# Kernel tuning notes

Hardware: AMD Instinct MI355X
Metric: run time of the kernel (lower is better)

## Reference

```python
import jax, jax.numpy as jnp
import numpy as np


def setup_inputs() -> dict:
    key = jax.random.key(0)
    B, L, H, D = 4, 4096, 8, 64
    sample_k = int(np.ceil(np.log(L)))  # factor=1 -> U_part = ceil(ln L_K) = 9
    k1, k2, k3, k4 = jax.random.split(key, 4)
    return {
        "queries": jax.random.normal(k1, (B, L, H, D), jnp.float32),
        "keys": jax.random.normal(k2, (B, L, H, D), jnp.float32),
        "values": jax.random.normal(k3, (B, L, H, D), jnp.float32),
        "index_sample": jax.random.randint(k4, (L, sample_k), 0, L),
    }


def _prob_attention(Q, K, V, index_sample):
    # Q, K, V: [B, H, L, D]
    B, H, L_K, D = K.shape
    L_Q = Q.shape[2]
    u = min(int(np.ceil(np.log(L_Q))), L_Q)  # n_top (static)

    # --- _prob_QK: sampled scores, sparsity measure M, top-u queries ---
    # gather sampled keys per query position: [B, H, L_Q, sample_k, D]
    K_sample = K[:, :, index_sample, :]
    QK_sample = jnp.einsum('bhld,bhlsd->bhls', Q, K_sample)  # [B,H,L_Q,S]
    M = QK_sample.max(axis=-1) - QK_sample.sum(axis=-1) / L_K  # [B,H,L_Q]
    _, M_top = jax.lax.top_k(M, u)  # [B,H,u] indices of top queries

    Q_reduce = jnp.take_along_axis(Q, M_top[..., None], axis=2)  # [B,H,u,D]
    scale = 1.0 / jnp.sqrt(jnp.asarray(D, Q.dtype))
    scores = jnp.einsum('bhud,bhkd->bhuk', Q_reduce, K) * scale  # [B,H,u,L_K]

    # --- initial context (mask_flag=False): mean of V over keys ---
    context = jnp.broadcast_to(V.mean(axis=2, keepdims=True), (B, H, L_Q, D))

    # --- update context at the top-u query positions ---
    attn = jax.nn.softmax(scores, axis=-1)  # [B,H,u,L_K]
    ctx_top = jnp.einsum('bhuk,bhkd->bhud', attn, V)  # [B,H,u,D]
    b_idx = jnp.arange(B)[:, None, None]
    h_idx = jnp.arange(H)[None, :, None]
    context = context.at[b_idx, h_idx, M_top].set(ctx_top)
    return context, attn


def reference(queries, keys, values, index_sample):
    # inputs: [B, L, H, D] -> internal [B, H, L, D]
    Q = queries.transpose(0, 2, 1, 3)
    K = keys.transpose(0, 2, 1, 3)
    V = values.transpose(0, 2, 1, 3)
    context, attn = _prob_attention(Q, K, V, index_sample)
    return context.transpose(0, 2, 1, 3), attn
```

## Files before the change

kernel.cpp:

```cpp
#include <hip/hip_runtime.h>
#include <math.h>

#define B_ 4
#define L_ 4096
#define H_ 8
#define D_ 64
#define S_ 9
#define U_ 9
#define VC_ 64
#define NC_ 32
#define CC_ 16
#define TKC_ 8

#define MBLK_ 2048
#define FILLBLK_ 8192

__device__ __forceinline__ float dot4(const float4& a, const float4& b) {
    return a.x * b.x + a.y * b.y + a.z * b.z + a.w * b.w;
}

__global__ void kernel_M_vmean(const float* __restrict__ Q, const float* __restrict__ K,
                               const int* __restrict__ idx, float* __restrict__ M,
                               const float* __restrict__ V, float* __restrict__ vpart) {
    if (blockIdx.x >= MBLK_) {
        int blk = blockIdx.x - MBLK_;
        int c = blk & (VC_ - 1), b = blk >> 6;
        int col = threadIdx.x & 127;
        int lp  = threadIdx.x >> 7;
        const int CHUNK = L_ / VC_;
        const float4* base = (const float4*)(V + (size_t)b * L_ * H_ * D_);
        float4 acc = make_float4(0.f, 0.f, 0.f, 0.f);
        for (int l = c * CHUNK + lp; l < (c + 1) * CHUNK; l += 2) {
            float4 v = base[(size_t)l * 128 + col];
            acc.x += v.x; acc.y += v.y; acc.z += v.z; acc.w += v.w;
        }
        __shared__ float4 red[256];
        red[threadIdx.x] = acc;
        __syncthreads();
        if (lp == 0) {
            float4 o = red[threadIdx.x + 128];
            acc.x += o.x; acc.y += o.y; acc.z += o.z; acc.w += o.w;
            ((float4*)vpart)[(size_t)blk * 128 + col] = acc;
        }
        return;
    }
    int n = blockIdx.x;
    int x = n & 7, m = n >> 3;
    int chunk = m & 63;
    int bh = (m >> 6) * 8 + x;
    int h = bh & (H_ - 1), b = bh >> 3;
    int t = threadIdx.x;
    int j = t & 3;
    int l = chunk * 64 + (t >> 2);

    int ki[S_];
#pragma unroll
    for (int s = 0; s < S_; ++s) ki[s] = idx[l * S_ + s];

    const float4* qb = (const float4*)(Q + (size_t)((b * L_ + l) * H_ + h) * D_);
    float4 q[4];
#pragma unroll
    for (int c = 0; c < 4; ++c) q[c] = qb[j + 4 * c];

    float dot[S_];
#pragma unroll
    for (int r = 0; r < 3; ++r) {
        const float4* kb0 = (const float4*)(K + (size_t)((b * L_ + ki[3*r+0]) * H_ + h) * D_);
        const float4* kb1 = (const float4*)(K + (size_t)((b * L_ + ki[3*r+1]) * H_ + h) * D_);
        const float4* kb2 = (const float4*)(K + (size_t)((b * L_ + ki[3*r+2]) * H_ + h) * D_);
        float4 kv0[4], kv1[4], kv2[4];
#pragma unroll
        for (int c = 0; c < 4; ++c) {
            kv0[c] = kb0[j + 4 * c];
            kv1[c] = kb1[j + 4 * c];
            kv2[c] = kb2[j + 4 * c];
        }
        float a0 = 0.f, a1 = 0.f, a2 = 0.f;
#pragma unroll
        for (int c = 0; c < 4; ++c) {
            a0 += dot4(q[c], kv0[c]);
            a1 += dot4(q[c], kv1[c]);
            a2 += dot4(q[c], kv2[c]);
        }
        dot[3*r+0] = a0; dot[3*r+1] = a1; dot[3*r+2] = a2;
    }
#pragma unroll
    for (int s = 0; s < S_; ++s) {
        dot[s] += __shfl_xor(dot[s], 1);
        dot[s] += __shfl_xor(dot[s], 2);
    }
    if (j == 0) {
        float mx = -INFINITY, sm = 0.f;
#pragma unroll
        for (int s = 0; s < S_; ++s) { mx = fmaxf(mx, dot[s]); sm += dot[s]; }
        M[((size_t)bh << 12) + l] = mx - sm * (1.0f / (float)L_);
    }
}

#define CSWAP(a, b)                                                          \
    if (v[b] > v[a] || (v[b] == v[a] && id[b] < id[a])) {                    \
        float tv = v[a]; v[a] = v[b]; v[b] = tv;                             \
        int ti = id[a]; id[a] = id[b]; id[b] = ti;                           \
    }

__global__ void kernel_topk1(const float* __restrict__ M,
                             float* __restrict__ cand_v, int* __restrict__ cand_i) {
    int bh = blockIdx.x >> 3;
    int chunk = blockIdx.x & (TKC_ - 1);
    int lane = threadIdx.x;
    const float* Ms = M + ((size_t)bh << 12);

    float v[8]; int id[8];
#pragma unroll
    for (int c = 0; c < 8; ++c) {
        int gi = chunk * 512 + lane + 64 * c;
        v[c] = Ms[gi]; id[c] = gi;
    }
    CSWAP(0,1) CSWAP(2,3) CSWAP(4,5) CSWAP(6,7)
    CSWAP(0,2) CSWAP(1,3) CSWAP(4,6) CSWAP(5,7)
    CSWAP(1,2) CSWAP(5,6)
    CSWAP(0,4) CSWAP(1,5) CSWAP(2,6) CSWAP(3,7)
    CSWAP(2,4) CSWAP(3,5)
    CSWAP(1,2) CSWAP(3,4) CSWAP(5,6)

    float* cv = cand_v + (size_t)blockIdx.x * U_;
    int*   ci = cand_i + (size_t)blockIdx.x * U_;
#pragma unroll
    for (int r = 0; r < U_; ++r) {
        float bv = v[0]; int bi = id[0];
#pragma unroll
        for (int off = 1; off < 64; off <<= 1) {
            float ov = __shfl_xor(bv, off);
            int   oi = __shfl_xor(bi, off);
            if (ov > bv || (ov == bv && oi < bi)) { bv = ov; bi = oi; }
        }
        if (lane == 0) { cv[r] = bv; ci[r] = bi; }
        if (id[0] == bi) {
#pragma unroll
            for (int c = 0; c < 7; ++c) { v[c] = v[c+1]; id[c] = id[c+1]; }
            v[7] = -INFINITY; id[7] = 0x7fffffff;
        }
    }
}

__global__ void kernel_small(const float* __restrict__ cand_v, const int* __restrict__ cand_i,
                             int* __restrict__ Mtop, const float* __restrict__ vpart,
                             float* __restrict__ vmean) {
    if (blockIdx.x >= 32) {
        int bh = blockIdx.x - 32;
        int h = bh & (H_ - 1), b = bh >> 3;
        int d = threadIdx.x;
        float s = 0.0f;
        for (int c = 0; c < VC_; ++c)
            s += vpart[(size_t)(b * VC_ + c) * (H_ * D_) + h * D_ + d];
        vmean[bh * D_ + d] = s * (1.0f / (float)L_);
        return;
    }
    int bh = blockIdx.x;
    int lane = threadIdx.x;
    const float* cv = cand_v + (size_t)bh * (TKC_ * U_);
    const int*   ci = cand_i + (size_t)bh * (TKC_ * U_);

    float v[2]; int id[2];
    v[0] = cv[lane]; id[0] = ci[lane];
    if (lane < TKC_ * U_ - 64) { v[1] = cv[64 + lane]; id[1] = ci[64 + lane]; }
    else { v[1] = -INFINITY; id[1] = 0x7fffffff; }
    CSWAP(0,1)

#pragma unroll
    for (int r = 0; r < U_; ++r) {
        float bv = v[0]; int bi = id[0];
#pragma unroll
        for (int off = 1; off < 64; off <<= 1) {
            float ov = __shfl_xor(bv, off);
            int   oi = __shfl_xor(bi, off);
            if (ov > bv || (ov == bv && oi < bi)) { bv = ov; bi = oi; }
        }
        if (lane == 0) Mtop[bh * U_ + r] = bi;
        if (id[0] == bi) { v[0] = v[1]; id[0] = id[1]; v[1] = -INFINITY; id[1] = 0x7fffffff; }
    }
}

__global__ void kernel_fill_scores(float* __restrict__ out, const float* __restrict__ vmean,
                                   const float* __restrict__ Q, const float* __restrict__ K,
                                   const int* __restrict__ Mtop, float* __restrict__ raw) {
    if (blockIdx.x < FILLBLK_) {
        int i = blockIdx.x * 256 + threadIdx.x;
        int d4 = i & 15;
        int h  = (i >> 4) & (H_ - 1);
        int b  = i >> (4 + 3 + 12);
        ((float4*)out)[i] = ((const float4*)vmean)[(b * H_ + h) * 16 + d4];
        return;
    }
    int n = blockIdx.x - FILLBLK_;
    int x = n & 7, m = n >> 3;
    int chunk = m & (NC_ - 1);
    int bh = (m >> 5) * 8 + x;
    int h = bh & (H_ - 1), b = bh >> 3;
    int k0 = chunk * (L_ / NC_);

    __shared__ float qs[U_][D_];
    int t = threadIdx.x;
    if (t < 144) {
        int u = t / 16, c = t & 15;
        int l = Mtop[bh * U_ + u];
        ((float4*)qs[u])[c] =
            ((const float4*)(Q + (size_t)((b * L_ + l) * H_ + h) * D_))[c];
    }
    __syncthreads();

    int j = t & 3, g = t >> 2;
#pragma unroll
    for (int kk = 0; kk < 2; ++kk) {
        int k = k0 + g + 64 * kk;
        const float4* kb = (const float4*)(K + (size_t)((b * L_ + k) * H_ + h) * D_);
        float4 kv[4];
#pragma unroll
        for (int c = 0; c < 4; ++c) kv[c] = kb[j + 4 * c];
#pragma unroll
        for (int u = 0; u < U_; ++u) {
            float acc = 0.0f;
#pragma unroll
            for (int c = 0; c < 4; ++c)
                acc += dot4(((const float4*)qs[u])[j + 4 * c], kv[c]);
            acc += __shfl_xor(acc, 1);
            acc += __shfl_xor(acc, 2);
            if (j == 0) raw[((size_t)bh * U_ + u) * L_ + k] = acc * 0.125f;
        }
    }
}

__global__ void kernel_softmax(float* __restrict__ attn) {
    int row = blockIdx.x;
    float4* a = (float4*)(attn + (size_t)row * L_);
    int t = threadIdx.x;

    float4 v[4];
    float mx = -INFINITY;
#pragma unroll
    for (int i = 0; i < 4; ++i) {
        v[i] = a[t + 256 * i];
        mx = fmaxf(mx, fmaxf(fmaxf(v[i].x, v[i].y), fmaxf(v[i].z, v[i].w)));
    }
    __shared__ float red[256];
    __shared__ float bmax, bsum;
    red[t] = mx;
    __syncthreads();
    for (int off = 128; off > 0; off >>= 1) {
        if (t < off) red[t] = fmaxf(red[t], red[t + off]);
        __syncthreads();
    }
    if (t == 0) bmax = red[0];
    __syncthreads();

    float mm = bmax, sum = 0.0f;
#pragma unroll
    for (int i = 0; i < 4; ++i) {
        v[i].x = expf(v[i].x - mm); v[i].y = expf(v[i].y - mm);
        v[i].z = expf(v[i].z - mm); v[i].w = expf(v[i].w - mm);
        sum += v[i].x + v[i].y + v[i].z + v[i].w;
    }
    red[t] = sum;
    __syncthreads();
    for (int off = 128; off > 0; off >>= 1) {
        if (t < off) red[t] += red[t + off];
        __syncthreads();
    }
    if (t == 0) bsum = red[0];
    __syncthreads();

    float inv = 1.0f / bsum;
#pragma unroll
    for (int i = 0; i < 4; ++i) {
        v[i].x *= inv; v[i].y *= inv; v[i].z *= inv; v[i].w *= inv;
        a[t + 256 * i] = v[i];
    }
}

__global__ void kernel_ctxf(const float* __restrict__ attn, const float* __restrict__ V,
                            float* __restrict__ cpart) {
    int n = blockIdx.x;
    int x = n & 7, m = n >> 3;
    int chunk = m & (CC_ - 1);
    int bh = (m >> 4) * 8 + x;
    int h = bh & (H_ - 1), b = bh >> 3;
    int k0 = chunk * (L_ / CC_);

    int t = threadIdx.x;
    int g = t >> 6, lane = t & 63;
    int kl = lane >> 4, d4 = lane & 15;
    const float* abase = attn + (size_t)bh * U_ * L_;

    float4 acc[U_];
#pragma unroll
    for (int u = 0; u < U_; ++u) acc[u] = make_float4(0.f, 0.f, 0.f, 0.f);

    for (int i = 0; i < 16; ++i) {
        int k = k0 + (g * 4 + kl) + 16 * i;
        float4 vv = *(const float4*)(V + (size_t)((b * L_ + k) * H_ + h) * D_ + 4 * d4);
        float av[U_];
#pragma unroll
        for (int u = 0; u < U_; ++u) av[u] = abase[(size_t)u * L_ + k];
#pragma unroll
        for (int u = 0; u < U_; ++u) {
            acc[u].x += av[u] * vv.x; acc[u].y += av[u] * vv.y;
            acc[u].z += av[u] * vv.z; acc[u].w += av[u] * vv.w;
        }
    }
#pragma unroll
    for (int u = 0; u < U_; ++u) {
        acc[u].x += __shfl_xor(acc[u].x, 16); acc[u].y += __shfl_xor(acc[u].y, 16);
        acc[u].z += __shfl_xor(acc[u].z, 16); acc[u].w += __shfl_xor(acc[u].w, 16);
        acc[u].x += __shfl_xor(acc[u].x, 32); acc[u].y += __shfl_xor(acc[u].y, 32);
        acc[u].z += __shfl_xor(acc[u].z, 32); acc[u].w += __shfl_xor(acc[u].w, 32);
    }
    __shared__ float4 red[U_][4][16];
    if (kl == 0) {
#pragma unroll
        for (int u = 0; u < U_; ++u) red[u][g][d4] = acc[u];
    }
    __syncthreads();
    if (t < U_ * 16) {
        int u = t >> 4, dd = t & 15;
        float4 s0 = red[u][0][dd], s1 = red[u][1][dd];
        float4 s2 = red[u][2][dd], s3 = red[u][3][dd];
        float4 s = make_float4(s0.x + s1.x + s2.x + s3.x, s0.y + s1.y + s2.y + s3.y,
                               s0.z + s1.z + s2.z + s3.z, s0.w + s1.w + s2.w + s3.w);
        ((float4*)cpart)[((size_t)(bh * CC_ + chunk) * U_ + u) * 16 + dd] = s;
    }
}

__global__ void kernel_ctx2(const float* __restrict__ cpart, const int* __restrict__ Mtop,
                            float* __restrict__ out) {
    int row = blockIdx.x;
    int u = row % U_, bh = row / U_;
    int h = bh & (H_ - 1), b = bh >> 3;
    int d = threadIdx.x;
    float s = 0.0f;
#pragma unroll
    for (int c = 0; c < CC_; ++c)
        s += cpart[((size_t)(bh * CC_ + c) * U_ + u) * 64 + d];
    int l = Mtop[bh * U_ + u];
    out[(size_t)((b * L_ + l) * H_ + h) * D_ + d] = s;
}

extern "C" void kernel_launch(void* const* d_in, const int* in_sizes, int n_in,
                              void* d_out, int out_size, void* d_ws, size_t ws_size,
                              hipStream_t stream) {
    const float* Q   = (const float*)d_in[0];
    const float* K   = (const float*)d_in[1];
    const float* V   = (const float*)d_in[2];
    const int*   idx = (const int*)d_in[3];

    float* ctx_out  = (float*)d_out;
    float* attn_out = (float*)d_out + (size_t)B_ * L_ * H_ * D_;

    float* M      = (float*)d_ws;
    float* vpart  = M + (size_t)B_ * H_ * L_;
    float* vmean  = vpart + (size_t)B_ * VC_ * H_ * D_;
    float* cpart  = vmean + B_ * H_ * D_;
    float* cand_v = cpart + (size_t)32 * CC_ * U_ * 64;
    int*   cand_i = (int*)(cand_v + 32 * TKC_ * U_);
    int*   Mtop   = cand_i + 32 * TKC_ * U_;

    kernel_M_vmean<<<MBLK_ + B_ * VC_, 256, 0, stream>>>(Q, K, idx, M, V, vpart);
    kernel_topk1<<<B_ * H_ * TKC_, 64, 0, stream>>>(M, cand_v, cand_i);
    kernel_small<<<64, 64, 0, stream>>>(cand_v, cand_i, Mtop, vpart, vmean);
    kernel_fill_scores<<<FILLBLK_ + 32 * NC_, 256, 0, stream>>>(ctx_out, vmean, Q, K, Mtop, attn_out);
    kernel_softmax<<<B_ * H_ * U_, 256, 0, stream>>>(attn_out);
    kernel_ctxf<<<32 * CC_, 256, 0, stream>>>(attn_out, V, cpart);
    kernel_ctx2<<<B_ * H_ * U_, 64, 0, stream>>>(cpart, Mtop, ctx_out);
}
```

Before: 232.0 us.

## Split sampled-QK per sample, fuse softmax normalize into ctx, atomically scatter context

The M computation now gives each sampled key its own thread group, writing raw dot products to a workspace. The top-k kernel then reduces them to max minus sum. Softmax is split into a stats pass that writes row max and inverse sum, and the exp/normalize step moves into the context kernel. That kernel writes the normalized attention back, stages it in shared memory, and atomically adds partial contexts into the output, removing the ctx2 reduction kernel. The fill kernel now zeroes the top-u rows so the atomics accumulate from zero. Costs are extra dot-product traffic in the workspace, a 9-way Mtop compare per fill thread, and float atomics, which make the summation order nondeterministic.

```diff
diff --git a/kernel.cpp b/kernel.cpp
--- a/kernel.cpp
+++ b/kernel.cpp
@@ -12,16 +12,16 @@
 #define CC_ 16
 #define TKC_ 8
 
-#define MBLK_ 2048
+#define MBLK_ 18432
 #define FILLBLK_ 8192
 
 __device__ __forceinline__ float dot4(const float4& a, const float4& b) {
     return a.x * b.x + a.y * b.y + a.z * b.z + a.w * b.w;
 }
 
-__global__ void kernel_M_vmean(const float* __restrict__ Q, const float* __restrict__ K,
-                               const int* __restrict__ idx, float* __restrict__ M,
-                               const float* __restrict__ V, float* __restrict__ vpart) {
+__global__ void kernel_Mv(const float* __restrict__ Q, const float* __restrict__ K,
+                          const int* __restrict__ idx, float* __restrict__ dots,
+                          const float* __restrict__ V, float* __restrict__ vpart) {
     if (blockIdx.x >= MBLK_) {
         int blk = blockIdx.x - MBLK_;
         int c = blk & (VC_ - 1), b = blk >> 6;
@@ -46,55 +46,25 @@
     }
     int n = blockIdx.x;
     int x = n & 7, m = n >> 3;
-    int chunk = m & 63;
-    int bh = (m >> 6) * 8 + x;
+    int bhi = m / 576, blk = m - bhi * 576;
+    int bh = bhi * 8 + x;
     int h = bh & (H_ - 1), b = bh >> 3;
     int t = threadIdx.x;
     int j = t & 3;
-    int l = chunk * 64 + (t >> 2);
-
-    int ki[S_];
-#pragma unroll
-    for (int s = 0; s < S_; ++s) ki[s] = idx[l * S_ + s];
-
+    int G = blk * 64 + (t >> 2);
+    int s = G >> 12;
+    int l = G & (L_ - 1);
+
+    int ki = idx[l * S_ + s];
     const float4* qb = (const float4*)(Q + (size_t)((b * L_ + l) * H_ + h) * D_);
-    float4 q[4];
-#pragma unroll
-    for (int c = 0; c < 4; ++c) q[c] = qb[j + 4 * c];
-
-    float dot[S_];
-#pragma unroll
-    for (int r = 0; r < 3; ++r) {
-        const float4* kb0 = (const float4*)(K + (size_t)((b * L_ + ki[3*r+0]) * H_ + h) * D_);
-        const float4* kb1 = (const float4*)(K + (size_t)((b * L_ + ki[3*r+1]) * H_ + h) * D_);
-        const float4* kb2 = (const float4*)(K + (size_t)((b * L_ + ki[3*r+2]) * H_ + h) * D_);
-        float4 kv0[4], kv1[4], kv2[4];
-#pragma unroll
-        for (int c = 0; c < 4; ++c) {
-            kv0[c] = kb0[j + 4 * c];
-            kv1[c] = kb1[j + 4 * c];
-            kv2[c] = kb2[j + 4 * c];
-        }
-        float a0 = 0.f, a1 = 0.f, a2 = 0.f;
-#pragma unroll
-        for (int c = 0; c < 4; ++c) {
-            a0 += dot4(q[c], kv0[c]);
-            a1 += dot4(q[c], kv1[c]);
-            a2 += dot4(q[c], kv2[c]);
-        }
-        dot[3*r+0] = a0; dot[3*r+1] = a1; dot[3*r+2] = a2;
-    }
-#pragma unroll
-    for (int s = 0; s < S_; ++s) {
-        dot[s] += __shfl_xor(dot[s], 1);
-        dot[s] += __shfl_xor(dot[s], 2);
-    }
-    if (j == 0) {
-        float mx = -INFINITY, sm = 0.f;
-#pragma unroll
-        for (int s = 0; s < S_; ++s) { mx = fmaxf(mx, dot[s]); sm += dot[s]; }
-        M[((size_t)bh << 12) + l] = mx - sm * (1.0f / (float)L_);
-    }
+    const float4* kb = (const float4*)(K + (size_t)((b * L_ + ki) * H_ + h) * D_);
+
+    float acc = 0.0f;
+#pragma unroll
+    for (int c = 0; c < 4; ++c) acc += dot4(qb[j + 4 * c], kb[j + 4 * c]);
+    acc += __shfl_xor(acc, 1);
+    acc += __shfl_xor(acc, 2);
+    if (j == 0) dots[((size_t)bh * S_ + s) * L_ + l] = acc;
 }
 
 #define CSWAP(a, b)                                                          \
@@ -103,18 +73,25 @@
         int ti = id[a]; id[a] = id[b]; id[b] = ti;                           \
     }
 
-__global__ void kernel_topk1(const float* __restrict__ M,
+__global__ void kernel_topk1(const float* __restrict__ dots,
                              float* __restrict__ cand_v, int* __restrict__ cand_i) {
     int bh = blockIdx.x >> 3;
     int chunk = blockIdx.x & (TKC_ - 1);
     int lane = threadIdx.x;
-    const float* Ms = M + ((size_t)bh << 12);
+    const float* db = dots + (size_t)bh * S_ * L_;
 
     float v[8]; int id[8];
 #pragma unroll
     for (int c = 0; c < 8; ++c) {
         int gi = chunk * 512 + lane + 64 * c;
-        v[c] = Ms[gi]; id[c] = gi;
+        float mx = -INFINITY, sm = 0.0f;
+#pragma unroll
+        for (int s = 0; s < S_; ++s) {
+            float d = db[(size_t)s * L_ + gi];
+            mx = fmaxf(mx, d); sm += d;
+        }
+        v[c] = mx - sm * (1.0f / (float)L_);
+        id[c] = gi;
     }
     CSWAP(0,1) CSWAP(2,3) CSWAP(4,5) CSWAP(6,7)
     CSWAP(0,2) CSWAP(1,3) CSWAP(4,6) CSWAP(5,7)
@@ -188,8 +165,15 @@
         int i = blockIdx.x * 256 + threadIdx.x;
         int d4 = i & 15;
         int h  = (i >> 4) & (H_ - 1);
-        int b  = i >> (4 + 3 + 12);
-        ((float4*)out)[i] = ((const float4*)vmean)[(b * H_ + h) * 16 + d4];
+        int l  = (i >> 7) & (L_ - 1);
+        int b  = i >> 19;
+        int bh = b * H_ + h;
+        bool top = false;
+#pragma unroll
+        for (int u = 0; u < U_; ++u) top |= (Mtop[bh * U_ + u] == l);
+        float4 w = top ? make_float4(0.f, 0.f, 0.f, 0.f)
+                       : ((const float4*)vmean)[bh * 16 + d4];
+        ((float4*)out)[i] = w;
         return;
     }
     int n = blockIdx.x - FILLBLK_;
@@ -230,9 +214,10 @@
     }
 }
 
-__global__ void kernel_softmax(float* __restrict__ attn) {
+__global__ void kernel_stats(const float* __restrict__ raw,
+                             float* __restrict__ smax, float* __restrict__ sinv) {
     int row = blockIdx.x;
-    float4* a = (float4*)(attn + (size_t)row * L_);
+    const float4* a = (const float4*)(raw + (size_t)row * L_);
     int t = threadIdx.x;
 
     float4 v[4];
@@ -243,7 +228,7 @@
         mx = fmaxf(mx, fmaxf(fmaxf(v[i].x, v[i].y), fmaxf(v[i].z, v[i].w)));
     }
     __shared__ float red[256];
-    __shared__ float bmax, bsum;
+    __shared__ float bmax;
     red[t] = mx;
     __syncthreads();
     for (int off = 128; off > 0; off >>= 1) {
@@ -255,56 +240,55 @@
 
     float mm = bmax, sum = 0.0f;
 #pragma unroll
-    for (int i = 0; i < 4; ++i) {
-        v[i].x = expf(v[i].x - mm); v[i].y = expf(v[i].y - mm);
-        v[i].z = expf(v[i].z - mm); v[i].w = expf(v[i].w - mm);
-        sum += v[i].x + v[i].y + v[i].z + v[i].w;
-    }
+    for (int i = 0; i < 4; ++i)
+        sum += expf(v[i].x - mm) + expf(v[i].y - mm) +
+               expf(v[i].z - mm) + expf(v[i].w - mm);
     red[t] = sum;
     __syncthreads();
     for (int off = 128; off > 0; off >>= 1) {
         if (t < off) red[t] += red[t + off];
         __syncthreads();
     }
-    if (t == 0) bsum = red[0];
-    __syncthreads();
-
-    float inv = 1.0f / bsum;
-#pragma unroll
-    for (int i = 0; i < 4; ++i) {
-        v[i].x *= inv; v[i].y *= inv; v[i].z *= inv; v[i].w *= inv;
-        a[t + 256 * i] = v[i];
-    }
-}
-
-__global__ void kernel_ctxf(const float* __restrict__ attn, const float* __restrict__ V,
-                            float* __restrict__ cpart) {
+    if (t == 0) { smax[row] = mm; sinv[row] = 1.0f / red[0]; }
+}
+
+__global__ void kernel_ctxf(float* __restrict__ attn, const float* __restrict__ V,
+                            const int* __restrict__ Mtop, const float* __restrict__ smax,
+                            const float* __restrict__ sinv, float* __restrict__ out) {
     int n = blockIdx.x;
     int x = n & 7, m = n >> 3;
     int chunk = m & (CC_ - 1);
     int bh = (m >> 4) * 8 + x;
     int h = bh & (H_ - 1), b = bh >> 3;
     int k0 = chunk * (L_ / CC_);
-
     int t = threadIdx.x;
+
+    __shared__ float sA[U_][256];
+    float* abase = attn + (size_t)bh * U_ * L_;
+#pragma unroll
+    for (int u = 0; u < U_; ++u) {
+        int row = bh * U_ + u;
+        float e = expf(abase[(size_t)u * L_ + k0 + t] - smax[row]) * sinv[row];
+        abase[(size_t)u * L_ + k0 + t] = e;
+        sA[u][t] = e;
+    }
+    __syncthreads();
+
     int g = t >> 6, lane = t & 63;
     int kl = lane >> 4, d4 = lane & 15;
-    const float* abase = attn + (size_t)bh * U_ * L_;
 
     float4 acc[U_];
 #pragma unroll
     for (int u = 0; u < U_; ++u) acc[u] = make_float4(0.f, 0.f, 0.f, 0.f);
 
     for (int i = 0; i < 16; ++i) {
-        int k = k0 + (g * 4 + kl) + 16 * i;
-        float4 vv = *(const float4*)(V + (size_t)((b * L_ + k) * H_ + h) * D_ + 4 * d4);
-        float av[U_];
-#pragma unroll
-        for (int u = 0; u < U_; ++u) av[u] = abase[(size_t)u * L_ + k];
+        int kloc = (g * 4 + kl) + 16 * i;
+        float4 vv = *(const float4*)(V + (size_t)((b * L_ + k0 + kloc) * H_ + h) * D_ + 4 * d4);
 #pragma unroll
         for (int u = 0; u < U_; ++u) {
-            acc[u].x += av[u] * vv.x; acc[u].y += av[u] * vv.y;
-            acc[u].z += av[u] * vv.z; acc[u].w += av[u] * vv.w;
+            float av = sA[u][kloc];
+            acc[u].x += av * vv.x; acc[u].y += av * vv.y;
+            acc[u].z += av * vv.z; acc[u].w += av * vv.w;
         }
     }
 #pragma unroll
@@ -324,24 +308,13 @@
         int u = t >> 4, dd = t & 15;
         float4 s0 = red[u][0][dd], s1 = red[u][1][dd];
         float4 s2 = red[u][2][dd], s3 = red[u][3][dd];
-        float4 s = make_float4(s0.x + s1.x + s2.x + s3.x, s0.y + s1.y + s2.y + s3.y,
-                               s0.z + s1.z + s2.z + s3.z, s0.w + s1.w + s2.w + s3.w);
-        ((float4*)cpart)[((size_t)(bh * CC_ + chunk) * U_ + u) * 16 + dd] = s;
-    }
-}
-
-__global__ void kernel_ctx2(const float* __restrict__ cpart, const int* __restrict__ Mtop,
-                            float* __restrict__ out) {
-    int row = blockIdx.x;
-    int u = row % U_, bh = row / U_;
-    int h = bh & (H_ - 1), b = bh >> 3;
-    int d = threadIdx.x;
-    float s = 0.0f;
-#pragma unroll
-    for (int c = 0; c < CC_; ++c)
-        s += cpart[((size_t)(bh * CC_ + c) * U_ + u) * 64 + d];
-    int l = Mtop[bh * U_ + u];
-    out[(size_t)((b * L_ + l) * H_ + h) * D_ + d] = s;
+        int lq = Mtop[bh * U_ + u];
+        float* o = out + (size_t)((b * L_ + lq) * H_ + h) * D_ + 4 * dd;
+        atomicAdd(o + 0, s0.x + s1.x + s2.x + s3.x);
+        atomicAdd(o + 1, s0.y + s1.y + s2.y + s3.y);
+        atomicAdd(o + 2, s0.z + s1.z + s2.z + s3.z);
+        atomicAdd(o + 3, s0.w + s1.w + s2.w + s3.w);
+    }
 }
 
 extern "C" void kernel_launch(void* const* d_in, const int* in_sizes, int n_in,
@@ -355,19 +328,19 @@
     float* ctx_out  = (float*)d_out;
     float* attn_out = (float*)d_out + (size_t)B_ * L_ * H_ * D_;
 
-    float* M      = (float*)d_ws;
-    float* vpart  = M + (size_t)B_ * H_ * L_;
+    float* dots   = (float*)d_ws;
+    float* vpart  = dots + (size_t)32 * S_ * L_;
     float* vmean  = vpart + (size_t)B_ * VC_ * H_ * D_;
-    float* cpart  = vmean + B_ * H_ * D_;
-    float* cand_v = cpart + (size_t)32 * CC_ * U_ * 64;
+    float* cand_v = vmean + B_ * H_ * D_;
     int*   cand_i = (int*)(cand_v + 32 * TKC_ * U_);
     int*   Mtop   = cand_i + 32 * TKC_ * U_;
-
-    kernel_M_vmean<<<MBLK_ + B_ * VC_, 256, 0, stream>>>(Q, K, idx, M, V, vpart);
-    kernel_topk1<<<B_ * H_ * TKC_, 64, 0, stream>>>(M, cand_v, cand_i);
+    float* smax   = (float*)(Mtop + 32 * U_);
+    float* sinv   = smax + 32 * U_;
+
+    kernel_Mv<<<MBLK_ + B_ * VC_, 256, 0, stream>>>(Q, K, idx, dots, V, vpart);
+    kernel_topk1<<<B_ * H_ * TKC_, 64, 0, stream>>>(dots, cand_v, cand_i);
     kernel_small<<<64, 64, 0, stream>>>(cand_v, cand_i, Mtop, vpart, vmean);
     kernel_fill_scores<<<FILLBLK_ + 32 * NC_, 256, 0, stream>>>(ctx_out, vmean, Q, K, Mtop, attn_out);
-    kernel_softmax<<<B_ * H_ * U_, 256, 0, stream>>>(attn_out);
-    kernel_ctxf<<<32 * CC_, 256, 0, stream>>>(attn_out, V, cpart);
-    kernel_ctx2<<<B_ * H_ * U_, 64, 0, stream>>>(cpart, Mtop, ctx_out);
-}
+    kernel_stats<<<B_ * H_ * U_, 256, 0, stream>>>(attn_out, smax, sinv);
+    kernel_ctxf<<<32 * CC_, 256, 0, stream>>>(attn_out, V, Mtop, smax, sinv, ctx_out);
+}
```

After: 243.7 us. +5.1%, slower.
